# Kernel tuning notes

Hardware: AMD Instinct MI355X
Metric: run time of the kernel (lower is better)

Reference implementation:

```python
import jax, jax.numpy as jnp
import numpy as np

N_NODES = 100000
N_EDGES = 3200000
D_IN = 96      # sum(latent_dim)
D_OUT = 32     # latent_dim[-1]
N_HEADS = 4
LEAKY_SLOPE = 0.2


def setup_inputs() -> dict:
    key = jax.random.key(0)
    k_x, k_w, k_a, k_src, k_dst = jax.random.split(key, 5)
    x = jax.random.normal(k_x, (N_NODES, D_IN), dtype=jnp.float32)
    # per-head GAT params (xavier-ish scale)
    W = jax.random.normal(k_w, (N_HEADS, D_IN, D_OUT), dtype=jnp.float32) * (1.414 / np.sqrt(D_IN))
    a = jax.random.normal(k_a, (N_HEADS, 2 * D_OUT), dtype=jnp.float32) * 0.1
    edge_src = jax.random.randint(k_src, (N_EDGES,), 0, N_NODES)
    edge_dst = jax.random.randint(k_dst, (N_EDGES,), 0, N_NODES)
    return {"x": x, "W": W, "a": a, "edge_src": edge_src, "edge_dst": edge_dst}


def reference(x, W, a, edge_src, edge_dst):
    # Multi-head sparse GAT layer (SpGraphAttentionLayer, concat=True, eval mode).
    N = x.shape[0]
    n_heads, _, d_out = W.shape
    outs = []
    for i in range(n_heads):  # small fixed head loop; data dims fully vectorized
        h = x @ W[i]                                   # [N, d_out]
        # a @ cat(h[src], h[dst]) == h[src]@a1 + h[dst]@a2 (avoids [E, 2*d_out] concat)
        s = h[edge_src] @ a[i, :d_out] + h[edge_dst] @ a[i, d_out:]   # [E]
        edge_e = jnp.exp(-jax.nn.leaky_relu(s, LEAKY_SLOPE))          # [E]
        # sparse_coo(edge, edge_e, [N,N]) @ h  ==  scatter-add of edge_e * h[dst] into src
        msg = edge_e[:, None] * h[edge_dst]                           # [E, d_out]
        h_prime = jax.ops.segment_sum(msg, edge_src, num_segments=N)  # [N, d_out]
        outs.append(jax.nn.elu(h_prime))
    return jnp.concatenate(outs, axis=1)  # [N, n_heads * d_out]
```

## Files before the change

### kernel.cpp

```cpp
#include <hip/hip_runtime.h>
#include <hip/hip_bf16.h>

#define DIN 96
#define DOUT 32
#define NH 4
#define DTOT 128
#define SLOPE 0.2f
#define NPBF 64
#define BSH 7
#define BNODES 128
#define MAXB 1024
#define EPB 4096
#define BCAP 5632

__device__ __forceinline__ unsigned int packbf2(float lo, float hi) {
    unsigned int a = __float_as_uint(lo), b = __float_as_uint(hi);
    a += 0x7fffu + ((a >> 16) & 1u);
    b += 0x7fffu + ((b >> 16) & 1u);
    return (a >> 16) | (b & 0xffff0000u);
}

__global__ __launch_bounds__(256) void feat_kernel(
    const float* __restrict__ x, const float* __restrict__ W,
    const float* __restrict__ a,
    unsigned int* __restrict__ hq,
    float2* __restrict__ usrc, float2* __restrict__ vdst,
    int* __restrict__ gcur, int n_nodes, int nb)
{
    __shared__ float Wlo[DIN * 64];
    __shared__ float Whi[DIN * 64];
    __shared__ float al[NH * 2 * DOUT];
    const int t = threadIdx.x;

    if (blockIdx.x == 0)
        for (int i = t; i < nb; i += 256) gcur[i] = i * BCAP;

    for (int i = t; i < DIN * DTOT; i += 256) {
        int k = i >> 7, c = i & 127;
        int head = c >> 5, j = c & 31;
        float w = W[head * (DIN * DOUT) + k * DOUT + j];
        int cbi = c >> 3, jj = c & 7;
        if (jj < 4) Wlo[(k << 6) + (cbi << 2) + jj] = w;
        else        Whi[(k << 6) + (cbi << 2) + (jj - 4)] = w;
    }
    for (int i = t; i < NH * 2 * DOUT; i += 256) al[i] = a[i];
    __syncthreads();

    const int cbi = t & 15;
    const int ng = t >> 4;
    const int node0 = blockIdx.x * NPBF;
    const int g0 = node0 + ng * 4;

    bool ok[4];
    const float* xp[4];
#pragma unroll
    for (int i = 0; i < 4; ++i) {
        ok[i] = (g0 + i) < n_nodes;
        xp[i] = x + (size_t)(g0 + i) * DIN;
    }

    float acc[4][8];
#pragma unroll
    for (int i = 0; i < 4; ++i)
#pragma unroll
        for (int j = 0; j < 8; ++j) acc[i][j] = 0.f;

    for (int k = 0; k < DIN; k += 4) {
        float4 xv[4];
#pragma unroll
        for (int i = 0; i < 4; ++i)
            xv[i] = ok[i] ? *(const float4*)(xp[i] + k)
                          : make_float4(0.f, 0.f, 0.f, 0.f);
#pragma unroll
        for (int kk = 0; kk < 4; ++kk) {
            const float4 wlo = *(const float4*)&Wlo[((k + kk) << 6) + (cbi << 2)];
            const float4 whi = *(const float4*)&Whi[((k + kk) << 6) + (cbi << 2)];
#pragma unroll
            for (int i = 0; i < 4; ++i) {
                const float xvv = (kk == 0) ? xv[i].x : (kk == 1) ? xv[i].y
                                 : (kk == 2) ? xv[i].z : xv[i].w;
                acc[i][0] = fmaf(xvv, wlo.x, acc[i][0]);
                acc[i][1] = fmaf(xvv, wlo.y, acc[i][1]);
                acc[i][2] = fmaf(xvv, wlo.z, acc[i][2]);
                acc[i][3] = fmaf(xvv, wlo.w, acc[i][3]);
                acc[i][4] = fmaf(xvv, whi.x, acc[i][4]);
                acc[i][5] = fmaf(xvv, whi.y, acc[i][5]);
                acc[i][6] = fmaf(xvv, whi.z, acc[i][6]);
                acc[i][7] = fmaf(xvv, whi.w, acc[i][7]);
            }
        }
    }

    const int head = cbi >> 2;
    const int j0 = (cbi & 3) << 3;
#pragma unroll
    for (int i = 0; i < 4; ++i) {
        float ps = 0.f, pd = 0.f;
#pragma unroll
        for (int j = 0; j < 8; ++j) {
            ps += acc[i][j] * al[head * 64 + j0 + j];
            pd += acc[i][j] * al[head * 64 + 32 + j0 + j];
        }
        ps += __shfl_xor(ps, 1); ps += __shfl_xor(ps, 2);
        pd += __shfl_xor(pd, 1); pd += __shfl_xor(pd, 2);
        const int g = g0 + i;
        if (ok[i]) {
            uint4 pk;
            pk.x = packbf2(acc[i][0], acc[i][1]);
            pk.y = packbf2(acc[i][2], acc[i][3]);
            pk.z = packbf2(acc[i][4], acc[i][5]);
            pk.w = packbf2(acc[i][6], acc[i][7]);
            *(uint4*)&hq[(size_t)g * 64 + (cbi << 2)] = pk;
            if ((cbi & 3) == 0) {
                usrc[g * NH + head] = make_float2(__expf(-ps), __expf(-SLOPE * ps));
                vdst[g * NH + head] = make_float2(__expf(-pd), __expf(-SLOPE * pd));
            }
        }
    }
}

__global__ __launch_bounds__(256) void binscatter_kernel(
    const int* __restrict__ esrc, const int* __restrict__ edst,
    int* __restrict__ gcur, unsigned int* __restrict__ binned,
    int n_edges, int nb)
{
    __shared__ int bc[MAXB];
    const int t = threadIdx.x;
    for (int i = t; i < nb; i += 256) bc[i] = 0;
    __syncthreads();

    const int base = blockIdx.x * EPB;
    const int end = min(base + EPB, n_edges);
    const bool full = (end - base) == EPB;

    int se[16], de[16];
    if (full) {
        const int4* s4p = (const int4*)(esrc + base);
        const int4* d4p = (const int4*)(edst + base);
#pragma unroll
        for (int j = 0; j < 4; ++j) {
            int4 s4 = s4p[j * 256 + t];
            int4 d4 = d4p[j * 256 + t];
            se[j * 4 + 0] = s4.x; se[j * 4 + 1] = s4.y;
            se[j * 4 + 2] = s4.z; se[j * 4 + 3] = s4.w;
            de[j * 4 + 0] = d4.x; de[j * 4 + 1] = d4.y;
            de[j * 4 + 2] = d4.z; de[j * 4 + 3] = d4.w;
        }
#pragma unroll
        for (int j = 0; j < 16; ++j)
            atomicAdd(&bc[se[j] >> BSH], 1);
    } else {
#pragma unroll
        for (int j = 0; j < 16; ++j) {
            const int e = base + j * 256 + t;
            se[j] = (e < end) ? esrc[e] : 0;
            de[j] = (e < end) ? edst[e] : 0;
            if (e < end) atomicAdd(&bc[se[j] >> BSH], 1);
        }
    }
    __syncthreads();

    for (int i = t; i < nb; i += 256) {
        int c = bc[i];
        bc[i] = (c > 0) ? atomicAdd(&gcur[i], c) : 0;
    }
    __syncthreads();

    if (full) {
#pragma unroll
        for (int j = 0; j < 16; ++j) {
            int s = se[j];
            int pos = atomicAdd(&bc[s >> BSH], 1);
            binned[pos] = ((unsigned int)(s & (BNODES - 1)) << 17) | (unsigned int)de[j];
        }
    } else {
#pragma unroll
        for (int j = 0; j < 16; ++j) {
            const int e = base + j * 256 + t;
            if (e < end) {
                int s = se[j];
                int pos = atomicAdd(&bc[s >> BSH], 1);
                binned[pos] = ((unsigned int)(s & (BNODES - 1)) << 17) | (unsigned int)de[j];
            }
        }
    }
}

__global__ __launch_bounds__(256) void binfine_kernel(
    const int* __restrict__ gcur,
    int* __restrict__ offs, int* __restrict__ deg,
    unsigned int* __restrict__ binned,
    int n_nodes)
{
    __shared__ unsigned int ebuf[BCAP];
    __shared__ int dcnt[BNODES];
    __shared__ int sc[BNODES];
    __shared__ int dcur[BNODES];
    const int t = threadIdx.x;
    const int b = blockIdx.x;
    const int base = b * BCAP;
    int cnt = gcur[b] - base;
    if (cnt > BCAP - 512) cnt = BCAP - 512;
    const int node0 = b << BSH;

    for (int i = t; i < cnt; i += 256) ebuf[i] = binned[base + i];
    if (t < BNODES) dcnt[t] = 0;
    __syncthreads();

    for (int i = t; i < cnt; i += 256)
        atomicAdd(&dcnt[ebuf[i] >> 17], 1);
    __syncthreads();

    int pd = 0;
    if (t < BNODES) { pd = (dcnt[t] + 3) & ~3; sc[t] = pd; }
    __syncthreads();
    for (int off = 1; off < BNODES; off <<= 1) {
        int v = 0;
        if (t < BNODES && t >= off) v = sc[t - off];
        __syncthreads();
        if (t < BNODES) sc[t] += v;
        __syncthreads();
    }
    if (t < BNODES) {
        int o = base + sc[t] - pd;
        dcur[t] = o;
        int node = node0 + t;
        if (node < n_nodes) { offs[node] = o; deg[node] = dcnt[t]; }
    }
    __syncthreads();

    for (int i = t; i < cnt; i += 256) {
        unsigned int w = ebuf[i];
        int pos = atomicAdd(&dcur[w >> 17], 1);
        binned[pos] = w & 0x1ffffu;
    }
}

__global__ __launch_bounds__(256) void gather_kernel(
    const int* __restrict__ slots, const int* __restrict__ offsets,
    const int* __restrict__ deg,
    const unsigned int* __restrict__ hv,
    const float2* __restrict__ usrc, const float2* __restrict__ vdst,
    float* __restrict__ out, int n_nodes)
{
    const int t = threadIdx.x;
    const int node = blockIdx.x * 4 + (t >> 6);
    if (node >= n_nodes) return;
    const int l = t & 63;
    const int head = l >> 4;
    const unsigned loff = (unsigned)l << 2;
    const unsigned hoff = (unsigned)head << 3;
    const char* __restrict__ hvb = (const char*)hv;
    const char* __restrict__ vdb = (const char*)vdst;
    const float2 u = usrc[(unsigned)node * 4u + head];
    const int beg = offsets[node];
    const int d = deg[node];

    float ax0 = 0.f, ay0 = 0.f, ax1 = 0.f, ay1 = 0.f;
    float ax2 = 0.f, ay2 = 0.f, ax3 = 0.f, ay3 = 0.f;

#define LDV(c) (*(const float2*)(vdb + ((((unsigned)(c)) << 5) + hoff)))
#define LDW(c) (*(const unsigned int*)(hvb + ((((unsigned)(c)) << 8) + loff)))
#define COMP(vv, ww, AX, AY) do {                                   \
        float e_ = fminf(u.x * (vv).x, u.y * (vv).y);               \
        AX = fmaf(e_, __uint_as_float((ww) << 16), AX);             \
        AY = fmaf(e_, __uint_as_float((ww) & 0xffff0000u), AY);     \
    } while (0)

    int k = 0;
    if (d >= 4) {
        int4 cA = *(const int4*)(slots + beg);
        float2 vA0 = LDV(cA.x), vA1 = LDV(cA.y), vA2 = LDV(cA.z), vA3 = LDV(cA.w);
        unsigned wA0 = LDW(cA.x), wA1 = LDW(cA.y), wA2 = LDW(cA.z), wA3 = LDW(cA.w);

        for (; k + 12 <= d; k += 8) {
            int4 cB = *(const int4*)(slots + beg + k + 4);
            float2 vB0 = LDV(cB.x), vB1 = LDV(cB.y), vB2 = LDV(cB.z), vB3 = LDV(cB.w);
            unsigned wB0 = LDW(cB.x), wB1 = LDW(cB.y), wB2 = LDW(cB.z), wB3 = LDW(cB.w);
            COMP(vA0, wA0, ax0, ay0); COMP(vA1, wA1, ax1, ay1);
            COMP(vA2, wA2, ax2, ay2); COMP(vA3, wA3, ax3, ay3);
            int4 cN = *(const int4*)(slots + beg + k + 8);
            vA0 = LDV(cN.x); vA1 = LDV(cN.y); vA2 = LDV(cN.z); vA3 = LDV(cN.w);
            wA0 = LDW(cN.x); wA1 = LDW(cN.y); wA2 = LDW(cN.z); wA3 = LDW(cN.w);
            COMP(vB0, wB0, ax0, ay0); COMP(vB1, wB1, ax1, ay1);
            COMP(vB2, wB2, ax2, ay2); COMP(vB3, wB3, ax3, ay3);
        }
        if (k + 8 <= d) {
            int4 cB = *(const int4*)(slots + beg + k + 4);
            float2 vB0 = LDV(cB.x), vB1 = LDV(cB.y), vB2 = LDV(cB.z), vB3 = LDV(cB.w);
            unsigned wB0 = LDW(cB.x), wB1 = LDW(cB.y), wB2 = LDW(cB.z), wB3 = LDW(cB.w);
            COMP(vA0, wA0, ax0, ay0); COMP(vA1, wA1, ax1, ay1);
            COMP(vA2, wA2, ax2, ay2); COMP(vA3, wA3, ax3, ay3);
            COMP(vB0, wB0, ax0, ay0); COMP(vB1, wB1, ax1, ay1);
            COMP(vB2, wB2, ax2, ay2); COMP(vB3, wB3, ax3, ay3);
            k += 8;
        } else {
            COMP(vA0, wA0, ax0, ay0); COMP(vA1, wA1, ax1, ay1);
            COMP(vA2, wA2, ax2, ay2); COMP(vA3, wA3, ax3, ay3);
            k += 4;
        }
    }
    for (; k < d; ++k) {
        int c = slots[beg + k];
        float2 v = LDV(c);
        unsigned w = LDW(c);
        COMP(v, w, ax0, ay0);
    }
#undef LDV
#undef LDW
#undef COMP

    float rx = (ax0 + ax1) + (ax2 + ax3);
    float ry = (ay0 + ay1) + (ay2 + ay3);
    rx = rx > 0.f ? rx : __expf(rx) - 1.f;
    ry = ry > 0.f ? ry : __expf(ry) - 1.f;
    ((float2*)out)[(unsigned)node * 64u + l] = make_float2(rx, ry);
}

extern "C" void kernel_launch(void* const* d_in, const int* in_sizes, int n_in,
                              void* d_out, int out_size, void* d_ws, size_t ws_size,
                              hipStream_t stream)
{
    const float* x  = (const float*)d_in[0];
    const float* W  = (const float*)d_in[1];
    const float* a  = (const float*)d_in[2];
    const int* esrc = (const int*)d_in[3];
    const int* edst = (const int*)d_in[4];
    const int n_nodes = in_sizes[0] / DIN;
    const int n_edges = in_sizes[3];
    float* out = (float*)d_out;

    const int nb = (n_nodes + BNODES - 1) >> BSH;

    unsigned int* hq = (unsigned int*)d_ws;
    float2* usrc = (float2*)(hq + (size_t)n_nodes * 64);
    float2* vdst = usrc + (size_t)n_nodes * NH;
    int* offs   = (int*)(vdst + (size_t)n_nodes * NH);
    int* deg    = offs + n_nodes;
    int* gcur   = deg + n_nodes;
    unsigned int* binned = (unsigned int*)(gcur + MAXB);

    feat_kernel<<<(n_nodes + NPBF - 1) / NPBF, 256, 0, stream>>>(
        x, W, a, hq, usrc, vdst, gcur, n_nodes, nb);

    binscatter_kernel<<<(n_edges + EPB - 1) / EPB, 256, 0, stream>>>(
        esrc, edst, gcur, binned, n_edges, nb);

    binfine_kernel<<<nb, 256, 0, stream>>>(
        gcur, offs, deg, binned, n_nodes);

    gather_kernel<<<(n_nodes + 3) / 4, 256, 0, stream>>>(
        (const int*)binned, offs, deg, hq, usrc, vdst, out, n_nodes);
}
```

Before: 423.3 us.

## Fuse feature and edge-binning kernels; merge fine binning with gather per bucket

Combines the feature transform and coarse edge-binning into one launch, interleaving binning blocks with feature blocks so the memory-bound and compute-bound work overlap. The fine per-node sort moves into shared memory inside a new bucket kernel that then gathers directly from the LDS slot list. This removes two launches and the global offs/deg arrays, and avoids writing sorted slots back to global memory. The cost is that each 512-thread block processes 128 nodes serially across 8 waves, which may reduce parallelism and latency hiding in the gather phase. A memset replaces the per-bin cursor initialisation.

```diff
diff --git a/kernel.cpp b/kernel.cpp
--- a/kernel.cpp
+++ b/kernel.cpp
@@ -20,20 +20,88 @@
     return (a >> 16) | (b & 0xffff0000u);
 }
 
-__global__ __launch_bounds__(256) void feat_kernel(
+__global__ __launch_bounds__(256) void prep_kernel(
     const float* __restrict__ x, const float* __restrict__ W,
     const float* __restrict__ a,
+    const int* __restrict__ esrc, const int* __restrict__ edst,
     unsigned int* __restrict__ hq,
     float2* __restrict__ usrc, float2* __restrict__ vdst,
-    int* __restrict__ gcur, int n_nodes, int nb)
+    int* __restrict__ gcur0, unsigned int* __restrict__ binned,
+    int n_nodes, int n_edges, int nb, int sblocks, int fblocks)
 {
     __shared__ float Wlo[DIN * 64];
     __shared__ float Whi[DIN * 64];
     __shared__ float al[NH * 2 * DOUT];
     const int t = threadIdx.x;
-
-    if (blockIdx.x == 0)
-        for (int i = t; i < nb; i += 256) gcur[i] = i * BCAP;
+    const int bid = (int)blockIdx.x;
+    const int q3 = bid / 3;
+    const int r3 = bid - q3 * 3;
+
+    if (r3 == 0 && q3 < sblocks) {
+        int* bc = (int*)Wlo;
+        for (int i = t; i < nb; i += 256) bc[i] = 0;
+        __syncthreads();
+
+        const int base = q3 * EPB;
+        const int end = min(base + EPB, n_edges);
+        const bool full = (end - base) == EPB;
+
+        int se[16], de[16];
+        if (full) {
+            const int4* s4p = (const int4*)(esrc + base);
+            const int4* d4p = (const int4*)(edst + base);
+#pragma unroll
+            for (int j = 0; j < 4; ++j) {
+                int4 s4 = s4p[j * 256 + t];
+                int4 d4 = d4p[j * 256 + t];
+                se[j * 4 + 0] = s4.x; se[j * 4 + 1] = s4.y;
+                se[j * 4 + 2] = s4.z; se[j * 4 + 3] = s4.w;
+                de[j * 4 + 0] = d4.x; de[j * 4 + 1] = d4.y;
+                de[j * 4 + 2] = d4.z; de[j * 4 + 3] = d4.w;
+            }
+#pragma unroll
+            for (int j = 0; j < 16; ++j)
+                atomicAdd(&bc[se[j] >> BSH], 1);
+        } else {
+#pragma unroll
+            for (int j = 0; j < 16; ++j) {
+                const int e = base + j * 256 + t;
+                se[j] = (e < end) ? esrc[e] : 0;
+                de[j] = (e < end) ? edst[e] : 0;
+                if (e < end) atomicAdd(&bc[se[j] >> BSH], 1);
+            }
+        }
+        __syncthreads();
+
+        for (int i = t; i < nb; i += 256) {
+            int c = bc[i];
+            bc[i] = (c > 0) ? (i * BCAP + atomicAdd(&gcur0[i], c)) : 0;
+        }
+        __syncthreads();
+
+        if (full) {
+#pragma unroll
+            for (int j = 0; j < 16; ++j) {
+                int s = se[j];
+                int pos = atomicAdd(&bc[s >> BSH], 1);
+                binned[pos] = ((unsigned int)(s & (BNODES - 1)) << 17) | (unsigned int)de[j];
+            }
+        } else {
+#pragma unroll
+            for (int j = 0; j < 16; ++j) {
+                const int e = base + j * 256 + t;
+                if (e < end) {
+                    int s = se[j];
+                    int pos = atomicAdd(&bc[s >> BSH], 1);
+                    binned[pos] = ((unsigned int)(s & (BNODES - 1)) << 17) | (unsigned int)de[j];
+                }
+            }
+        }
+        return;
+    }
+
+    const int fid = bid - min(q3 + (r3 ? 1 : 0), sblocks);
+    if (fid >= fblocks) return;
 
     for (int i = t; i < DIN * DTOT; i += 256) {
         int k = i >> 7, c = i & 127;
@@ -48,7 +116,7 @@
 
     const int cbi = t & 15;
     const int ng = t >> 4;
-    const int node0 = blockIdx.x * NPBF;
+    const int node0 = fid * NPBF;
     const int g0 = node0 + ng * 4;
 
     bool ok[4];
@@ -119,98 +187,29 @@
     }
 }
 
-__global__ __launch_bounds__(256) void binscatter_kernel(
-    const int* __restrict__ esrc, const int* __restrict__ edst,
-    int* __restrict__ gcur, unsigned int* __restrict__ binned,
-    int n_edges, int nb)
+__global__ __launch_bounds__(512) void bucket_kernel(
+    const int* __restrict__ gcur0,
+    const unsigned int* __restrict__ binned,
+    const unsigned int* __restrict__ hv,
+    const float2* __restrict__ usrc, const float2* __restrict__ vdst,
+    float* __restrict__ out, int n_nodes)
 {
-    __shared__ int bc[MAXB];
-    const int t = threadIdx.x;
-    for (int i = t; i < nb; i += 256) bc[i] = 0;
-    __syncthreads();
-
-    const int base = blockIdx.x * EPB;
-    const int end = min(base + EPB, n_edges);
-    const bool full = (end - base) == EPB;
-
-    int se[16], de[16];
-    if (full) {
-        const int4* s4p = (const int4*)(esrc + base);
-        const int4* d4p = (const int4*)(edst + base);
-#pragma unroll
-        for (int j = 0; j < 4; ++j) {
-            int4 s4 = s4p[j * 256 + t];
-            int4 d4 = d4p[j * 256 + t];
-            se[j * 4 + 0] = s4.x; se[j * 4 + 1] = s4.y;
-            se[j * 4 + 2] = s4.z; se[j * 4 + 3] = s4.w;
-            de[j * 4 + 0] = d4.x; de[j * 4 + 1] = d4.y;
-            de[j * 4 + 2] = d4.z; de[j * 4 + 3] = d4.w;
-        }
-#pragma unroll
-        for (int j = 0; j < 16; ++j)
-            atomicAdd(&bc[se[j] >> BSH], 1);
-    } else {
-#pragma unroll
-        for (int j = 0; j < 16; ++j) {
-            const int e = base + j * 256 + t;
-            se[j] = (e < end) ? esrc[e] : 0;
-            de[j] = (e < end) ? edst[e] : 0;
-            if (e < end) atomicAdd(&bc[se[j] >> BSH], 1);
-        }
-    }
-    __syncthreads();
-
-    for (int i = t; i < nb; i += 256) {
-        int c = bc[i];
-        bc[i] = (c > 0) ? atomicAdd(&gcur[i], c) : 0;
-    }
-    __syncthreads();
-
-    if (full) {
-#pragma unroll
-        for (int j = 0; j < 16; ++j) {
-            int s = se[j];
-            int pos = atomicAdd(&bc[s >> BSH], 1);
-            binned[pos] = ((unsigned int)(s & (BNODES - 1)) << 17) | (unsigned int)de[j];
-        }
-    } else {
-#pragma unroll
-        for (int j = 0; j < 16; ++j) {
-            const int e = base + j * 256 + t;
-            if (e < end) {
-                int s = se[j];
-                int pos = atomicAdd(&bc[s >> BSH], 1);
-                binned[pos] = ((unsigned int)(s & (BNODES - 1)) << 17) | (unsigned int)de[j];
-            }
-        }
-    }
-}
-
-__global__ __launch_bounds__(256) void binfine_kernel(
-    const int* __restrict__ gcur,
-    int* __restrict__ offs, int* __restrict__ deg,
-    unsigned int* __restrict__ binned,
-    int n_nodes)
-{
-    __shared__ unsigned int ebuf[BCAP];
+    __shared__ int slist[BCAP];
     __shared__ int dcnt[BNODES];
     __shared__ int sc[BNODES];
     __shared__ int dcur[BNODES];
     const int t = threadIdx.x;
-    const int b = blockIdx.x;
-    const int base = b * BCAP;
-    int cnt = gcur[b] - base;
+    const int b = (int)blockIdx.x;
+    const unsigned base = (unsigned)b * BCAP;
+    int cnt = gcur0[b];
     if (cnt > BCAP - 512) cnt = BCAP - 512;
     const int node0 = b << BSH;
 
-    for (int i = t; i < cnt; i += 256) ebuf[i] = binned[base + i];
     if (t < BNODES) dcnt[t] = 0;
     __syncthreads();
-
-    for (int i = t; i < cnt; i += 256)
-        atomicAdd(&dcnt[ebuf[i] >> 17], 1);
-    __syncthreads();
-
+    for (int i = t; i < cnt; i += 512)
+        atomicAdd(&dcnt[binned[base + i] >> 17], 1);
+    __syncthreads();
     int pd = 0;
     if (t < BNODES) { pd = (dcnt[t] + 3) & ~3; sc[t] = pd; }
     __syncthreads();
@@ -221,43 +220,22 @@
         if (t < BNODES) sc[t] += v;
         __syncthreads();
     }
-    if (t < BNODES) {
-        int o = base + sc[t] - pd;
-        dcur[t] = o;
-        int node = node0 + t;
-        if (node < n_nodes) { offs[node] = o; deg[node] = dcnt[t]; }
-    }
-    __syncthreads();
-
-    for (int i = t; i < cnt; i += 256) {
-        unsigned int w = ebuf[i];
+    if (t < BNODES) dcur[t] = sc[t] - pd;
+    __syncthreads();
+    for (int i = t; i < cnt; i += 512) {
+        unsigned int w = binned[base + i];
         int pos = atomicAdd(&dcur[w >> 17], 1);
-        binned[pos] = w & 0x1ffffu;
-    }
-}
-
-__global__ __launch_bounds__(256) void gather_kernel(
-    const int* __restrict__ slots, const int* __restrict__ offsets,
-    const int* __restrict__ deg,
-    const unsigned int* __restrict__ hv,
-    const float2* __restrict__ usrc, const float2* __restrict__ vdst,
-    float* __restrict__ out, int n_nodes)
-{
-    const int t = threadIdx.x;
-    const int node = blockIdx.x * 4 + (t >> 6);
-    if (node >= n_nodes) return;
+        slist[pos] = (int)(w & 0x1ffffu);
+    }
+    __syncthreads();
+
     const int l = t & 63;
     const int head = l >> 4;
     const unsigned loff = (unsigned)l << 2;
     const unsigned hoff = (unsigned)head << 3;
     const char* __restrict__ hvb = (const char*)hv;
     const char* __restrict__ vdb = (const char*)vdst;
-    const float2 u = usrc[(unsigned)node * 4u + head];
-    const int beg = offsets[node];
-    const int d = deg[node];
-
-    float ax0 = 0.f, ay0 = 0.f, ax1 = 0.f, ay1 = 0.f;
-    float ax2 = 0.f, ay2 = 0.f, ax3 = 0.f, ay3 = 0.f;
+    const int sub = t >> 6;
 
 #define LDV(c) (*(const float2*)(vdb + ((((unsigned)(c)) << 5) + hoff)))
 #define LDW(c) (*(const unsigned int*)(hvb + ((((unsigned)(c)) << 8) + loff)))
@@ -267,54 +245,64 @@
         AY = fmaf(e_, __uint_as_float((ww) & 0xffff0000u), AY);     \
     } while (0)
 
-    int k = 0;
-    if (d >= 4) {
-        int4 cA = *(const int4*)(slots + beg);
-        float2 vA0 = LDV(cA.x), vA1 = LDV(cA.y), vA2 = LDV(cA.z), vA3 = LDV(cA.w);
-        unsigned wA0 = LDW(cA.x), wA1 = LDW(cA.y), wA2 = LDW(cA.z), wA3 = LDW(cA.w);
-
-        for (; k + 12 <= d; k += 8) {
-            int4 cB = *(const int4*)(slots + beg + k + 4);
-            float2 vB0 = LDV(cB.x), vB1 = LDV(cB.y), vB2 = LDV(cB.z), vB3 = LDV(cB.w);
-            unsigned wB0 = LDW(cB.x), wB1 = LDW(cB.y), wB2 = LDW(cB.z), wB3 = LDW(cB.w);
-            COMP(vA0, wA0, ax0, ay0); COMP(vA1, wA1, ax1, ay1);
-            COMP(vA2, wA2, ax2, ay2); COMP(vA3, wA3, ax3, ay3);
-            int4 cN = *(const int4*)(slots + beg + k + 8);
-            vA0 = LDV(cN.x); vA1 = LDV(cN.y); vA2 = LDV(cN.z); vA3 = LDV(cN.w);
-            wA0 = LDW(cN.x); wA1 = LDW(cN.y); wA2 = LDW(cN.z); wA3 = LDW(cN.w);
-            COMP(vB0, wB0, ax0, ay0); COMP(vB1, wB1, ax1, ay1);
-            COMP(vB2, wB2, ax2, ay2); COMP(vB3, wB3, ax3, ay3);
-        }
-        if (k + 8 <= d) {
-            int4 cB = *(const int4*)(slots + beg + k + 4);
-            float2 vB0 = LDV(cB.x), vB1 = LDV(cB.y), vB2 = LDV(cB.z), vB3 = LDV(cB.w);
-            unsigned wB0 = LDW(cB.x), wB1 = LDW(cB.y), wB2 = LDW(cB.z), wB3 = LDW(cB.w);
-            COMP(vA0, wA0, ax0, ay0); COMP(vA1, wA1, ax1, ay1);
-            COMP(vA2, wA2, ax2, ay2); COMP(vA3, wA3, ax3, ay3);
-            COMP(vB0, wB0, ax0, ay0); COMP(vB1, wB1, ax1, ay1);
-            COMP(vB2, wB2, ax2, ay2); COMP(vB3, wB3, ax3, ay3);
-            k += 8;
-        } else {
-            COMP(vA0, wA0, ax0, ay0); COMP(vA1, wA1, ax1, ay1);
-            COMP(vA2, wA2, ax2, ay2); COMP(vA3, wA3, ax3, ay3);
-            k += 4;
-        }
-    }
-    for (; k < d; ++k) {
-        int c = slots[beg + k];
-        float2 v = LDV(c);
-        unsigned w = LDW(c);
-        COMP(v, w, ax0, ay0);
+    for (int q = 0; q < BNODES / 8; ++q) {
+        const int nd = q * 8 + sub;
+        const int node = node0 + nd;
+        if (node >= n_nodes) break;
+        const int d = dcnt[nd];
+        const int beg = dcur[nd] - d;
+        const float2 u = usrc[(unsigned)node * 4u + head];
+
+        float ax0 = 0.f, ay0 = 0.f, ax1 = 0.f, ay1 = 0.f;
+        float ax2 = 0.f, ay2 = 0.f, ax3 = 0.f, ay3 = 0.f;
+        int k = 0;
+        if (d >= 4) {
+            int4 cA = *(const int4*)&slist[beg];
+            float2 vA0 = LDV(cA.x), vA1 = LDV(cA.y), vA2 = LDV(cA.z), vA3 = LDV(cA.w);
+            unsigned wA0 = LDW(cA.x), wA1 = LDW(cA.y), wA2 = LDW(cA.z), wA3 = LDW(cA.w);
+
+            for (; k + 12 <= d; k += 8) {
+                int4 cB = *(const int4*)&slist[beg + k + 4];
+                float2 vB0 = LDV(cB.x), vB1 = LDV(cB.y), vB2 = LDV(cB.z), vB3 = LDV(cB.w);
+                unsigned wB0 = LDW(cB.x), wB1 = LDW(cB.y), wB2 = LDW(cB.z), wB3 = LDW(cB.w);
+                COMP(vA0, wA0, ax0, ay0); COMP(vA1, wA1, ax1, ay1);
+                COMP(vA2, wA2, ax2, ay2); COMP(vA3, wA3, ax3, ay3);
+                int4 cN = *(const int4*)&slist[beg + k + 8];
+                vA0 = LDV(cN.x); vA1 = LDV(cN.y); vA2 = LDV(cN.z); vA3 = LDV(cN.w);
+                wA0 = LDW(cN.x); wA1 = LDW(cN.y); wA2 = LDW(cN.z); wA3 = LDW(cN.w);
+                COMP(vB0, wB0, ax0, ay0); COMP(vB1, wB1, ax1, ay1);
+                COMP(vB2, wB2, ax2, ay2); COMP(vB3, wB3, ax3, ay3);
+            }
+            if (k + 8 <= d) {
+                int4 cB = *(const int4*)&slist[beg + k + 4];
+                float2 vB0 = LDV(cB.x), vB1 = LDV(cB.y), vB2 = LDV(cB.z), vB3 = LDV(cB.w);
+                unsigned wB0 = LDW(cB.x), wB1 = LDW(cB.y), wB2 = LDW(cB.z), wB3 = LDW(cB.w);
+                COMP(vA0, wA0, ax0, ay0); COMP(vA1, wA1, ax1, ay1);
+                COMP(vA2, wA2, ax2, ay2); COMP(vA3, wA3, ax3, ay3);
+                COMP(vB0, wB0, ax0, ay0); COMP(vB1, wB1, ax1, ay1);
+                COMP(vB2, wB2, ax2, ay2); COMP(vB3, wB3, ax3, ay3);
+                k += 8;
+            } else {
+                COMP(vA0, wA0, ax0, ay0); COMP(vA1, wA1, ax1, ay1);
+                COMP(vA2, wA2, ax2, ay2); COMP(vA3, wA3, ax3, ay3);
+                k += 4;
+            }
+        }
+        for (; k < d; ++k) {
+            int c = slist[beg + k];
+            float2 v = LDV(c);
+            unsigned w = LDW(c);
+            COMP(v, w, ax0, ay0);
+        }
+        float rx = (ax0 + ax1) + (ax2 + ax3);
+        float ry = (ay0 + ay1) + (ay2 + ay3);
+        rx = rx > 0.f ? rx : __expf(rx) - 1.f;
+        ry = ry > 0.f ? ry : __expf(ry) - 1.f;
+        ((float2*)out)[(unsigned)node * 64u + l] = make_float2(rx, ry);
     }
 #undef LDV
 #undef LDW
 #undef COMP
-
-    float rx = (ax0 + ax1) + (ax2 + ax3);
-    float ry = (ay0 + ay1) + (ay2 + ay3);
-    rx = rx > 0.f ? rx : __expf(rx) - 1.f;
-    ry = ry > 0.f ? ry : __expf(ry) - 1.f;
-    ((float2*)out)[(unsigned)node * 64u + l] = make_float2(rx, ry);
 }
 
 extern "C" void kernel_launch(void* const* d_in, const int* in_sizes, int n_in,
@@ -335,20 +323,20 @@
     unsigned int* hq = (unsigned int*)d_ws;
     float2* usrc = (float2*)(hq + (size_t)n_nodes * 64);
     float2* vdst = usrc + (size_t)n_nodes * NH;
-    int* offs   = (int*)(vdst + (size_t)n_nodes * NH);
-    int* deg    = offs + n_nodes;
-    int* gcur   = deg + n_nodes;
-    unsigned int* binned = (unsigned int*)(gcur + MAXB);
-
-    feat_kernel<<<(n_nodes + NPBF - 1) / NPBF, 256, 0, stream>>>(
-        x, W, a, hq, usrc, vdst, gcur, n_nodes, nb);
-
-    binscatter_kernel<<<(n_edges + EPB - 1) / EPB, 256, 0, stream>>>(
-        esrc, edst, gcur, binned, n_edges, nb);
-
-    binfine_kernel<<<nb, 256, 0, stream>>>(
-        gcur, offs, deg, binned, n_nodes);
-
-    gather_kernel<<<(n_nodes + 3) / 4, 256, 0, stream>>>(
-        (const int*)binned, offs, deg, hq, usrc, vdst, out, n_nodes);
+    int* gcur0  = (int*)(vdst + (size_t)n_nodes * NH);
+    unsigned int* binned = (unsigned int*)(gcur0 + MAXB);
+
+    hipMemsetAsync(gcur0, 0, MAXB * sizeof(int), stream);
+
+    const int SB = (n_edges + EPB - 1) / EPB;
+    const int FB = (n_nodes + NPBF - 1) / NPBF;
+    int grid = SB + FB;
+    if (grid < 3 * SB - 2) grid = 3 * SB - 2;
+
+    prep_kernel<<<grid, 256, 0, stream>>>(
+        x, W, a, esrc, edst, hq, usrc, vdst, gcur0, binned,
+        n_nodes, n_edges, nb, SB, FB);
+
+    bucket_kernel<<<nb, 512, 0, stream>>>(
+        gcur0, binned, hq, usrc, vdst, out, n_nodes);
 }
```

After: 418.7 us. No clear change (-1.1%).
